# Performance work log

Measured on AMD Instinct MI355X. Metric: run time of the kernel, lower is better.

The kernel has to match this reference:

```python
import jax, jax.numpy as jnp
import numpy as np

B, L, D, F, E, K = 2, 2048, 1024, 4096, 8, 2


def setup_inputs() -> dict:
    key = jax.random.key(0)
    ks = jax.random.split(key, 8)
    s = 0.02
    return {
        "x": jax.random.normal(ks[0], (B, L, D), dtype=jnp.float32),
        "Wg": jax.random.normal(ks[1], (D, E), dtype=jnp.float32) * s,
        "bg": jnp.zeros((E,), dtype=jnp.float32),
        "W1": jax.random.normal(ks[2], (E, D, F), dtype=jnp.float32) * s,
        "b1": jnp.zeros((E, F), dtype=jnp.float32),
        "W2": jax.random.normal(ks[3], (E, F, D), dtype=jnp.float32) * s,
        "b2": jnp.zeros((E, D), dtype=jnp.float32),
    }


def reference(x, Wg, bg, W1, b1, W2, b2):
    num_experts = Wg.shape[1]
    gate_scores = x @ Wg + bg                                # [B,L,E]
    topk_scores, topk_ids = jax.lax.top_k(gate_scores, K)    # [B,L,K]
    topk_weights = jax.nn.softmax(topk_scores, axis=-1)      # [B,L,K]
    gate_probs = jax.nn.softmax(gate_scores, axis=-1)        # [B,L,E]

    onehot = jax.nn.one_hot(topk_ids, num_experts, dtype=x.dtype)  # [B,L,K,E]
    expert_mask = onehot.sum(axis=2)                         # [B,L,E]
    freq = expert_mask.mean(axis=(0, 1))                     # [E]
    prob_mean = gate_probs.mean(axis=(0, 1))                 # [E]
    load_balance_loss = num_experts * jnp.sum(freq * prob_mean)

    # combine weight per token per expert (0 if expert not selected)
    combine = jnp.sum(onehot * topk_weights[..., None], axis=2)    # [B,L,E]

    # dense dispatch: run every expert FFN on all tokens, weight & combine
    h = jnp.einsum('bld,edf->belf', x, W1) + b1[None, :, None, :]  # [B,E,L,F]
    h = jax.nn.gelu(h, approximate=False)                          # exact GELU (torch default)
    y = jnp.einsum('belf,efd->beld', h, W2) + b2[None, :, None, :] # [B,E,L,D]
    out = jnp.einsum('ble,beld->bld', combine, y)                  # [B,L,D]
    return out, load_balance_loss
```

## Files before the change

kernel.cpp:

```cpp
#include <hip/hip_runtime.h>
#include <hip/hip_bf16.h>
#include <cstdint>
#include <cstddef>

#define B_ 2
#define L_ 2048
#define D_ 1024
#define F_ 4096
#define E_ 8
#define NTOK 4096
#define MAXROWS 9216
#define MAXMT 72

typedef __hip_bfloat16 bf16;
typedef __attribute__((ext_vector_type(8))) short short8;
typedef __attribute__((ext_vector_type(4))) float floatx4;

typedef const __attribute__((address_space(1))) uint32_t* gptr_t;
typedef __attribute__((address_space(3))) uint32_t* lptr_t;

__device__ __forceinline__ void async_load16(const bf16* gp, bf16* lp) {
    __builtin_amdgcn_global_load_lds((gptr_t)(const void*)gp, (lptr_t)(void*)lp, 16, 0, 0);
}

__device__ __forceinline__ uint16_t bfbits(bf16 h) {
    union { bf16 b; uint16_t u; } v; v.b = h; return v.u;
}
__device__ __forceinline__ uint32_t pack2(float a, float b) {
    return (uint32_t)bfbits(__float2bfloat16(a)) | ((uint32_t)bfbits(__float2bfloat16(b)) << 16);
}
__device__ __forceinline__ float ublo(uint32_t u){ return __uint_as_float(u << 16); }
__device__ __forceinline__ float ubhi(uint32_t u){ return __uint_as_float(u & 0xffff0000u); }

__device__ __forceinline__ float fast_gelu(float x) {
    float x2 = x * x;
    float z = x * fmaf(0.1029432f, x2, 2.3022081f);
    z = fminf(z, 120.f);
    float u = __builtin_amdgcn_exp2f(z);
    return x * u * __builtin_amdgcn_rcpf(1.f + u);
}

__global__ __launch_bounds__(256) void gate_kernel(
    const float* __restrict__ x, const float* __restrict__ Wg,
    const float* __restrict__ bg, float* __restrict__ psum_pad,
    uint32_t* __restrict__ top_ids, float* __restrict__ top_w)
{
    __shared__ float psum_l[E_];
    int t = threadIdx.x;
    if (t < E_) psum_l[t] = 0.f;
    __syncthreads();

    int wave = t >> 6, lane = t & 63;
    for (int j = 0; j < 4; ++j) {
        int token = blockIdx.x * 16 + wave * 4 + j;
        const float* xr = x + (size_t)token * D_;

        float acc[E_];
#pragma unroll
        for (int e = 0; e < E_; ++e) acc[e] = 0.f;
#pragma unroll
        for (int i = 0; i < 4; ++i) {
            int d = lane * 4 + 256 * i;
            float4 xv = *(const float4*)(xr + d);
            const float* xs = &xv.x;
#pragma unroll
            for (int jj = 0; jj < 4; ++jj) {
                const float4* wr4 = (const float4*)(Wg + (size_t)(d + jj) * E_);
                float4 wa = wr4[0], wb = wr4[1];
                float xvj = xs[jj];
                acc[0] += xvj * wa.x;  acc[1] += xvj * wa.y;
                acc[2] += xvj * wa.z;  acc[3] += xvj * wa.w;
                acc[4] += xvj * wb.x;  acc[5] += xvj * wb.y;
                acc[6] += xvj * wb.z;  acc[7] += xvj * wb.w;
            }
        }
#pragma unroll
        for (int off = 32; off >= 1; off >>= 1) {
#pragma unroll
            for (int e = 0; e < E_; ++e) acc[e] += __shfl_xor(acc[e], off, 64);
        }
        if (lane == 0) {
            float s[E_];
#pragma unroll
            for (int e = 0; e < E_; ++e) s[e] = acc[e] + bg[e];
            int i0 = 0;
#pragma unroll
            for (int e = 1; e < E_; ++e) if (s[e] > s[i0]) i0 = e;
            int i1 = -1;
#pragma unroll
            for (int e = 0; e < E_; ++e) {
                if (e == i0) continue;
                if (i1 < 0 || s[e] > s[i1]) i1 = e;
            }
            float e1 = expf(s[i1] - s[i0]);
            float w0 = 1.f / (1.f + e1);
            float w1 = e1 * w0;
            top_ids[token] = (uint32_t)i0 | ((uint32_t)i1 << 8);
            top_w[token]        = w0;
            top_w[NTOK + token] = w1;

            float mx = s[i0], p[E_], sum = 0.f;
#pragma unroll
            for (int e = 0; e < E_; ++e) { p[e] = expf(s[e] - mx); sum += p[e]; }
            float inv = 1.f / sum;
#pragma unroll
            for (int e = 0; e < E_; ++e) atomicAdd(&psum_l[e], p[e] * inv);
        }
    }
    __syncthreads();
    if (t < E_) atomicAdd(&psum_pad[t * 32], psum_l[t]);
}

__global__ __launch_bounds__(256) void compact_kernel(
    const uint32_t* __restrict__ top_ids, const float* __restrict__ top_w,
    int* __restrict__ cnt, int* __restrict__ tok_list, float* __restrict__ w_list,
    int* __restrict__ rowid)
{
    int e = blockIdx.x;
    int t = threadIdx.x, wave = t >> 6, lane = t & 63;
    __shared__ int wcnt[4];
    int base = 0;
    for (int r0 = 0; r0 < NTOK; r0 += 256) {
        int token = r0 + t;
        uint32_t ids = top_ids[token];
        int slot = -1;
        if ((int)(ids & 255u) == e) slot = 0;
        else if ((int)((ids >> 8) & 255u) == e) slot = 1;
        unsigned long long mask = __ballot(slot >= 0);
        int lpos = __popcll(mask & ((1ull << lane) - 1ull));
        if (lane == 0) wcnt[wave] = (int)__popcll(mask);
        __syncthreads();
        int woff = 0, tot = 0;
#pragma unroll
        for (int w2 = 0; w2 < 4; ++w2) { if (w2 < wave) woff += wcnt[w2]; tot += wcnt[w2]; }
        if (slot >= 0) {
            int pos = base + woff + lpos;
            tok_list[e*NTOK + pos] = token;
            w_list[e*NTOK + pos]   = top_w[slot*NTOK + token];
            rowid[slot*NTOK + token] = (e << 13) | pos;
        }
        base += tot;
        __syncthreads();
    }
    if (t == 0) cnt[e] = base;
}

__global__ void finalize_gate_kernel(const int* __restrict__ cnt, const float* __restrict__ psum_pad,
                                     int* __restrict__ off, float* __restrict__ loss_out,
                                     int* __restrict__ mt_map, int* __restrict__ mt_hdr)
{
    int o = 0; float Ls = 0.f; int g = 0;
    for (int e = 0; e < E_; ++e) {
        off[e] = o;
        int mt = (cnt[e] + 127) >> 7;
        for (int m = 0; m < mt; ++m) mt_map[g++] = (e << 8) | m;
        o += mt << 7;
        Ls += (float)cnt[e] * psum_pad[e * 32];
    }
    mt_hdr[0] = g;
    mt_hdr[1] = (g + 7) >> 3;
    loss_out[0] = (float)E_ * Ls / ((float)NTOK * (float)NTOK);
}

__global__ __launch_bounds__(256) void transpose_bf16_kernel(
    const float* __restrict__ in, bf16* __restrict__ outp, int R, int C)
{
    int tilesR = R >> 6, tilesC = C >> 6;
    int per = tilesR * tilesC;
    int bx = blockIdx.x;
    int e  = bx / per; int r2 = bx % per;
    int tr = r2 / tilesC, tc = r2 % tilesC;
    int r0 = tr << 6, c0 = tc << 6;
    const float* ip = in  + (size_t)e * R * C;
    bf16*        op = outp + (size_t)e * R * C;

    __shared__ uint32_t T[64][36];
    int t = threadIdx.x;
    int rp = t >> 4;
    int c4 = (t & 15) * 4;

#pragma unroll
    for (int it = 0; it < 2; ++it) {
        int pr = rp + 16 * it;
        const float* p = ip + (size_t)(r0 + 2*pr) * C + c0 + c4;
        float4 a = *(const float4*)(p);
        float4 b = *(const float4*)(p + C);
        T[c4+0][pr] = pack2(a.x, b.x);
        T[c4+1][pr] = pack2(a.y, b.y);
        T[c4+2][pr] = pack2(a.z, b.z);
        T[c4+3][pr] = pack2(a.w, b.w);
    }
    __syncthreads();

    int s     = t & 7;
    int cbase = t >> 3;
#pragma unroll
    for (int pass = 0; pass < 2; ++pass) {
        int cc = cbase + 32 * pass;
        uint4 u = *(const uint4*)&T[cc][4*s];
        *(uint4*)(op + (size_t)(c0 + cc) * R + r0 + 8*s) = u;
    }
}

__global__ __launch_bounds__(256) void gather_kernel(
    const float* __restrict__ x, const int* __restrict__ cnt, const int* __restrict__ off,
    const int* __restrict__ tok_list, bf16* __restrict__ Xg)
{
    int bx = blockIdx.x;
    int e  = bx >> 12;
    int i  = bx & 4095;
    if (i >= cnt[e]) return;
    int tok = tok_list[e*NTOK + i];
    size_t row = (size_t)(off[e] + i);
    int t = threadIdx.x;
    float4 v = *(const float4*)(x + (size_t)tok * D_ + t*4);
    uint2 uu;
    uu.x = pack2(v.x, v.y);
    uu.y = pack2(v.z, v.w);
    *(uint2*)(Xg + row * D_ + t*4) = uu;
}

__global__ __launch_bounds__(256) void gemm1_kernel(
    const bf16* __restrict__ Xg, const bf16* __restrict__ W1t,
    const float* __restrict__ b1, const int* __restrict__ cnt,
    const int* __restrict__ off, bf16* __restrict__ H)
{
    int bx = blockIdx.x;
    int e  = bx >> 10;
    int r2 = bx & 1023;
    int mtile = r2 >> 5, ntile = r2 & 31;
    int n = cnt[e];
    if (mtile * 128 >= n) return;
    int row0 = off[e] + mtile * 128;
    int f0 = ntile * 128;

    __shared__ bf16 As[128*64];
    __shared__ bf16 Bs[128*64];

    int t = threadIdx.x;
    int wave = t >> 6, lane = t & 63;
    int wm = wave & 1, wn = wave >> 1;
    int q = lane >> 4, ln = lane & 15;
    int sm = lane >> 3, sc = lane & 7;

    const bf16* Abase = Xg  + (size_t)row0 * D_;
    const bf16* Bbase = W1t + ((size_t)e * F_ + f0) * D_;

    floatx4 acc[4][4];
#pragma unroll
    for (int mt = 0; mt < 4; ++mt)
#pragma unroll
        for (int nt = 0; nt < 4; ++nt) acc[mt][nt] = {0.f, 0.f, 0.f, 0.f};

    for (int kt = 0; kt < D_; kt += 64) {
        __syncthreads();
#pragma unroll
        for (int i = 0; i < 4; ++i) {
            int g = wave*4 + i;
            int m = g*8 + sm;
            int ca = sc ^ (m & 7);
            async_load16(Abase + (size_t)m * D_ + kt + ca*8, &As[g*512]);
            async_load16(Bbase + (size_t)m * D_ + kt + ca*8, &Bs[g*512]);
        }
        __syncthreads();
#pragma unroll
        for (int kk = 0; kk < 2; ++kk) {
            short8 av[4], bv[4];
#pragma unroll
            for (int mt = 0; mt < 4; ++mt) {
                int r = wm*64 + mt*16 + ln;
                int cs = (kk*4 + q) ^ (r & 7);
                av[mt] = *(const short8*)&As[r*64 + cs*8];
            }
#pragma unroll
            for (int nt = 0; nt < 4; ++nt) {
                int r = wn*64 + nt*16 + ln;
                int cs = (kk*4 + q) ^ (r & 7);
                bv[nt] = *(const short8*)&Bs[r*64 + cs*8];
            }
#pragma unroll
            for (int mt = 0; mt < 4; ++mt)
#pragma unroll
                for (int nt = 0; nt < 4; ++nt)
                    acc[mt][nt] = __builtin_amdgcn_mfma_f32_16x16x32_bf16(av[mt], bv[nt], acc[mt][nt], 0, 0, 0);
        }
    }

#pragma unroll
    for (int nt = 0; nt < 4; ++nt) {
        int f = f0 + wn*64 + nt*16 + ln;
        float b1v = b1[(size_t)e * F_ + f];
#pragma unroll
        for (int mt = 0; mt < 4; ++mt) {
            int rl = wm*64 + mt*16 + q*4;
#pragma unroll
            for (int r = 0; r < 4; ++r) {
                float v = acc[mt][nt][r] + b1v;
                H[(size_t)(row0 + rl + r) * F_ + f] = __float2bfloat16(fast_gelu(v));
            }
        }
    }
}

__global__ __launch_bounds__(256) void gemm2_kernel(
    const bf16* __restrict__ H, const bf16* __restrict__ W2t,
    const float* __restrict__ b2, const int* __restrict__ cnt, const int* __restrict__ off,
    const int* __restrict__ mt_map, const int* __restrict__ mt_hdr,
    bf16* __restrict__ Y)
{
    int bx = blockIdx.x;
    int k  = bx & 7;
    int j  = bx >> 3;
    int jj = j >> 3;
    int ntile = j & 7;
    int nmt = mt_hdr[0], qc = mt_hdr[1];
    if (jj >= qc) return;
    int mt = k * qc + jj;
    if (mt >= nmt) return;
    int em = mt_map[mt];
    int e = em >> 8, mtile = em & 255;
    int n = cnt[e];
    int row0 = off[e] + mtile * 128;
    int d0 = ntile * 128;

    __shared__ bf16 As[2][128*64];
    __shared__ bf16 Bs[2][128*64];

    int t = threadIdx.x;
    int wave = t >> 6, lane = t & 63;
    int wm = wave & 1, wn = wave >> 1;
    int q = lane >> 4, ln = lane & 15;
    int sm = lane >> 3, sc = lane & 7;

    const bf16* Abase = H   + (size_t)row0 * F_;
    const bf16* Bbase = W2t + ((size_t)e * D_ + d0) * F_;

    int g0 = wave*4;
    auto stage = [&](int b, int kt) {
#pragma unroll
        for (int i = 0; i < 4; ++i) {
            int g = g0 + i;
            int m = g*8 + sm;
            int ca = sc ^ (m & 7);
            async_load16(Abase + (size_t)m * F_ + kt + ca*8, &As[b][g*512]);
            async_load16(Bbase + (size_t)m * F_ + kt + ca*8, &Bs[b][g*512]);
        }
    };

    floatx4 acc[4][4];
#pragma unroll
    for (int mt2 = 0; mt2 < 4; ++mt2)
#pragma unroll
        for (int nt = 0; nt < 4; ++nt) acc[mt2][nt] = {0.f, 0.f, 0.f, 0.f};

    stage(0, 0);
    __syncthreads();
    int cur = 0;

    for (int kt = 0; kt < F_; kt += 64) {
        if (kt + 64 < F_) stage(cur ^ 1, kt + 64);
#pragma unroll
        for (int kk = 0; kk < 2; ++kk) {
            short8 av[4], bv[4];
#pragma unroll
            for (int mt2 = 0; mt2 < 4; ++mt2) {
                int r = wm*64 + mt2*16 + ln;
                int cs = (kk*4 + q) ^ (r & 7);
                av[mt2] = *(const short8*)&As[cur][r*64 + cs*8];
            }
#pragma unroll
            for (int nt = 0; nt < 4; ++nt) {
                int r = wn*64 + nt*16 + ln;
                int cs = (kk*4 + q) ^ (r & 7);
                bv[nt] = *(const short8*)&Bs[cur][r*64 + cs*8];
            }
#pragma unroll
            for (int mt2 = 0; mt2 < 4; ++mt2)
#pragma unroll
                for (int nt = 0; nt < 4; ++nt)
                    acc[mt2][nt] = __builtin_amdgcn_mfma_f32_16x16x32_bf16(av[mt2], bv[nt], acc[mt2][nt], 0, 0, 0);
        }
        __syncthreads();
        cur ^= 1;
    }

    float b2v[4];
#pragma unroll
    for (int nt = 0; nt < 4; ++nt)
        b2v[nt] = b2[(size_t)e * D_ + d0 + wn*64 + nt*16 + ln];

#pragma unroll
    for (int mt2 = 0; mt2 < 4; ++mt2) {
#pragma unroll
        for (int r = 0; r < 4; ++r) {
            int loc = wm*64 + mt2*16 + q*4 + r;
            int i = mtile*128 + loc;
            if (i < n) {
                bf16* yp = Y + (size_t)(row0 + loc) * D_ + d0;
#pragma unroll
                for (int nt = 0; nt < 4; ++nt)
                    yp[wn*64 + nt*16 + ln] = __float2bfloat16(acc[mt2][nt][r] + b2v[nt]);
            }
        }
    }
}

__global__ __launch_bounds__(256) void combine_kernel(
    const bf16* __restrict__ Y, const int* __restrict__ rowid,
    const float* __restrict__ top_w, const int* __restrict__ off,
    float* __restrict__ out)
{
    int tok = blockIdx.x;
    int t = threadIdx.x;
    int v0 = rowid[tok], v1 = rowid[NTOK + tok];
    float w0 = top_w[tok], w1 = top_w[NTOK + tok];
    size_t r0 = (size_t)(off[v0 >> 13] + (v0 & 8191));
    size_t r1 = (size_t)(off[v1 >> 13] + (v1 & 8191));
    uint2 a = *(const uint2*)(Y + r0 * D_ + t*4);
    uint2 b = *(const uint2*)(Y + r1 * D_ + t*4);
    float4 o;
    o.x = w0 * ublo(a.x) + w1 * ublo(b.x);
    o.y = w0 * ubhi(a.x) + w1 * ubhi(b.x);
    o.z = w0 * ublo(a.y) + w1 * ublo(b.y);
    o.w = w0 * ubhi(a.y) + w1 * ubhi(b.y);
    *(float4*)(out + (size_t)tok * D_ + t*4) = o;
}

extern "C" void kernel_launch(void* const* d_in, const int* in_sizes, int n_in,
                              void* d_out, int out_size, void* d_ws, size_t ws_size,
                              hipStream_t stream)
{
    const float* x  = (const float*)d_in[0];
    const float* Wg = (const float*)d_in[1];
    const float* bg = (const float*)d_in[2];
    const float* W1 = (const float*)d_in[3];
    const float* b1 = (const float*)d_in[4];
    const float* W2 = (const float*)d_in[5];
    const float* b2 = (const float*)d_in[6];
    float* out = (float*)d_out;

    char* ws = (char*)d_ws;
    int*      cnt      = (int*)(ws + 0);
    int*      off      = (int*)(ws + 128);
    int*      mt_map   = (int*)(ws + 256);
    int*      mt_hdr   = (int*)(ws + 576);
    float*    psum_pad = (float*)(ws + 1024);
    uint32_t* top_ids  = (uint32_t*)(ws + 8192);
    float*    top_w    = (float*)(ws + 8192 + 16384);
    int*      tok_list = (int*)(ws + 65536);
    float*    w_list   = (float*)(ws + 65536 + 131072);
    int*      rowid    = (int*)(ws + 327680);
    size_t o = 1u << 20;
    bf16*  W1t = (bf16*)(ws + o);  o += (size_t)E_ * D_ * F_ * 2;
    bf16*  W2t = (bf16*)(ws + o);  o += (size_t)E_ * F_ * D_ * 2;
    bf16*  Xg  = (bf16*)(ws + o);  o += (size_t)MAXROWS * D_ * 2;
    bf16*  H   = (bf16*)(ws + o);
    bf16*  Y   = Xg;

    hipMemsetAsync(ws + 1024, 0, 1024, stream);

    transpose_bf16_kernel<<<E_ * 16 * 64, 256, 0, stream>>>(W1, W1t, D_, F_);
    transpose_bf16_kernel<<<E_ * 64 * 16, 256, 0, stream>>>(W2, W2t, F_, D_);

    gate_kernel<<<256, 256, 0, stream>>>(x, Wg, bg, psum_pad, top_ids, top_w);
    compact_kernel<<<E_, 256, 0, stream>>>(top_ids, top_w, cnt, tok_list, w_list, rowid);
    finalize_gate_kernel<<<1, 1, 0, stream>>>(cnt, psum_pad, off, out + (size_t)NTOK * D_, mt_map, mt_hdr);
    gather_kernel<<<E_ * 4096, 256, 0, stream>>>(x, cnt, off, tok_list, Xg);

    gemm1_kernel<<<E_ * 32 * 32, 256, 0, stream>>>(Xg, W1t, b1, cnt, off, H);
    gemm2_kernel<<<MAXMT * 8, 256, 0, stream>>>(H, W2t, b2, cnt, off, mt_map, mt_hdr, Y);
    combine_kernel<<<NTOK, 256, 0, stream>>>(Y, rowid, top_w, off, out);
}
```

Measured before the change: 654.5 us.

## Add four-stage async LDS pipeline to both expert GEMMs and compact gemm1 grid

Both grouped GEMMs now keep four LDS buffers and issue async global-to-LDS loads three k-steps ahead. Explicit vmcnt waits and a single barrier per step replace the previous double-buffer or single-buffer schedule. gemm1 also takes the compacted m-tile map, so it launches only live tiles, interleaved across 8 slots the same way gemm2 does, instead of a fixed per-expert grid with early exits. Shared memory per block grows to 128KB, which limits occupancy to one block per CU, and the hand-counted vmcnt values depend on the exact number of loads per stage.

```diff
diff --git a/kernel.cpp b/kernel.cpp
--- a/kernel.cpp
+++ b/kernel.cpp
@@ -223,19 +223,25 @@
 __global__ __launch_bounds__(256) void gemm1_kernel(
     const bf16* __restrict__ Xg, const bf16* __restrict__ W1t,
     const float* __restrict__ b1, const int* __restrict__ cnt,
-    const int* __restrict__ off, bf16* __restrict__ H)
+    const int* __restrict__ off, const int* __restrict__ mt_map,
+    const int* __restrict__ mt_hdr, bf16* __restrict__ H)
 {
     int bx = blockIdx.x;
-    int e  = bx >> 10;
-    int r2 = bx & 1023;
-    int mtile = r2 >> 5, ntile = r2 & 31;
-    int n = cnt[e];
-    if (mtile * 128 >= n) return;
+    int k  = bx & 7;
+    int j  = bx >> 3;
+    int jj = j >> 5;
+    int ntile = j & 31;
+    int nmt = mt_hdr[0], qc = mt_hdr[1];
+    if (jj >= qc) return;
+    int mt = k * qc + jj;
+    if (mt >= nmt) return;
+    int em = mt_map[mt];
+    int e = em >> 8, mtile = em & 255;
     int row0 = off[e] + mtile * 128;
     int f0 = ntile * 128;
 
-    __shared__ bf16 As[128*64];
-    __shared__ bf16 Bs[128*64];
+    __shared__ bf16 As[4][128*64];
+    __shared__ bf16 Bs[4][128*64];
 
     int t = threadIdx.x;
     int wave = t >> 6, lane = t & 63;
@@ -246,56 +252,80 @@
     const bf16* Abase = Xg  + (size_t)row0 * D_;
     const bf16* Bbase = W1t + ((size_t)e * F_ + f0) * D_;
 
-    floatx4 acc[4][4];
-#pragma unroll
-    for (int mt = 0; mt < 4; ++mt)
-#pragma unroll
-        for (int nt = 0; nt < 4; ++nt) acc[mt][nt] = {0.f, 0.f, 0.f, 0.f};
-
-    for (int kt = 0; kt < D_; kt += 64) {
-        __syncthreads();
+    int g0 = wave*4;
+    auto stage = [&](int b, int kt) {
 #pragma unroll
         for (int i = 0; i < 4; ++i) {
-            int g = wave*4 + i;
+            int g = g0 + i;
             int m = g*8 + sm;
             int ca = sc ^ (m & 7);
-            async_load16(Abase + (size_t)m * D_ + kt + ca*8, &As[g*512]);
-            async_load16(Bbase + (size_t)m * D_ + kt + ca*8, &Bs[g*512]);
-        }
-        __syncthreads();
+            async_load16(Abase + (size_t)m * D_ + kt + ca*8, &As[b][g*512]);
+            async_load16(Bbase + (size_t)m * D_ + kt + ca*8, &Bs[b][g*512]);
+        }
+    };
+
+    floatx4 acc[4][4];
+#pragma unroll
+    for (int mt2 = 0; mt2 < 4; ++mt2)
+#pragma unroll
+        for (int nt = 0; nt < 4; ++nt) acc[mt2][nt] = {0.f, 0.f, 0.f, 0.f};
+
+    auto compute = [&](int b) {
 #pragma unroll
         for (int kk = 0; kk < 2; ++kk) {
             short8 av[4], bv[4];
 #pragma unroll
-            for (int mt = 0; mt < 4; ++mt) {
-                int r = wm*64 + mt*16 + ln;
+            for (int mt2 = 0; mt2 < 4; ++mt2) {
+                int r = wm*64 + mt2*16 + ln;
                 int cs = (kk*4 + q) ^ (r & 7);
-                av[mt] = *(const short8*)&As[r*64 + cs*8];
+                av[mt2] = *(const short8*)&As[b][r*64 + cs*8];
             }
 #pragma unroll
             for (int nt = 0; nt < 4; ++nt) {
                 int r = wn*64 + nt*16 + ln;
                 int cs = (kk*4 + q) ^ (r & 7);
-                bv[nt] = *(const short8*)&Bs[r*64 + cs*8];
-            }
-#pragma unroll
-            for (int mt = 0; mt < 4; ++mt)
+                bv[nt] = *(const short8*)&Bs[b][r*64 + cs*8];
+            }
+#pragma unroll
+            for (int mt2 = 0; mt2 < 4; ++mt2)
 #pragma unroll
                 for (int nt = 0; nt < 4; ++nt)
-                    acc[mt][nt] = __builtin_amdgcn_mfma_f32_16x16x32_bf16(av[mt], bv[nt], acc[mt][nt], 0, 0, 0);
-        }
-    }
+                    acc[mt2][nt] = __builtin_amdgcn_mfma_f32_16x16x32_bf16(av[mt2], bv[nt], acc[mt2][nt], 0, 0, 0);
+        }
+    };
+
+    const int NT = D_ / 64;
+    stage(0, 0); stage(1, 64); stage(2, 128);
+    for (int i = 0; i < NT - 3; ++i) {
+        asm volatile("s_waitcnt vmcnt(16)" ::: "memory");
+        __builtin_amdgcn_s_barrier();
+        __builtin_amdgcn_sched_barrier(0);
+        stage((i + 3) & 3, (i + 3) * 64);
+        compute(i & 3);
+    }
+    asm volatile("s_waitcnt vmcnt(16)" ::: "memory");
+    __builtin_amdgcn_s_barrier();
+    __builtin_amdgcn_sched_barrier(0);
+    compute((NT - 3) & 3);
+    asm volatile("s_waitcnt vmcnt(8)" ::: "memory");
+    __builtin_amdgcn_s_barrier();
+    __builtin_amdgcn_sched_barrier(0);
+    compute((NT - 2) & 3);
+    asm volatile("s_waitcnt vmcnt(0)" ::: "memory");
+    __builtin_amdgcn_s_barrier();
+    __builtin_amdgcn_sched_barrier(0);
+    compute((NT - 1) & 3);
 
 #pragma unroll
     for (int nt = 0; nt < 4; ++nt) {
         int f = f0 + wn*64 + nt*16 + ln;
         float b1v = b1[(size_t)e * F_ + f];
 #pragma unroll
-        for (int mt = 0; mt < 4; ++mt) {
-            int rl = wm*64 + mt*16 + q*4;
+        for (int mt2 = 0; mt2 < 4; ++mt2) {
+            int rl = wm*64 + mt2*16 + q*4;
 #pragma unroll
             for (int r = 0; r < 4; ++r) {
-                float v = acc[mt][nt][r] + b1v;
+                float v = acc[mt2][nt][r] + b1v;
                 H[(size_t)(row0 + rl + r) * F_ + f] = __float2bfloat16(fast_gelu(v));
             }
         }
@@ -323,8 +353,8 @@
     int row0 = off[e] + mtile * 128;
     int d0 = ntile * 128;
 
-    __shared__ bf16 As[2][128*64];
-    __shared__ bf16 Bs[2][128*64];
+    __shared__ bf16 As[4][128*64];
+    __shared__ bf16 Bs[4][128*64];
 
     int t = threadIdx.x;
     int wave = t >> 6, lane = t & 63;
@@ -353,12 +383,7 @@
 #pragma unroll
         for (int nt = 0; nt < 4; ++nt) acc[mt2][nt] = {0.f, 0.f, 0.f, 0.f};
 
-    stage(0, 0);
-    __syncthreads();
-    int cur = 0;
-
-    for (int kt = 0; kt < F_; kt += 64) {
-        if (kt + 64 < F_) stage(cur ^ 1, kt + 64);
+    auto compute = [&](int b) {
 #pragma unroll
         for (int kk = 0; kk < 2; ++kk) {
             short8 av[4], bv[4];
@@ -366,13 +391,13 @@
             for (int mt2 = 0; mt2 < 4; ++mt2) {
                 int r = wm*64 + mt2*16 + ln;
                 int cs = (kk*4 + q) ^ (r & 7);
-                av[mt2] = *(const short8*)&As[cur][r*64 + cs*8];
+                av[mt2] = *(const short8*)&As[b][r*64 + cs*8];
             }
 #pragma unroll
             for (int nt = 0; nt < 4; ++nt) {
                 int r = wn*64 + nt*16 + ln;
                 int cs = (kk*4 + q) ^ (r & 7);
-                bv[nt] = *(const short8*)&Bs[cur][r*64 + cs*8];
+                bv[nt] = *(const short8*)&Bs[b][r*64 + cs*8];
             }
 #pragma unroll
             for (int mt2 = 0; mt2 < 4; ++mt2)
@@ -380,9 +405,29 @@
                 for (int nt = 0; nt < 4; ++nt)
                     acc[mt2][nt] = __builtin_amdgcn_mfma_f32_16x16x32_bf16(av[mt2], bv[nt], acc[mt2][nt], 0, 0, 0);
         }
-        __syncthreads();
-        cur ^= 1;
-    }
+    };
+
+    const int NT = F_ / 64;
+    stage(0, 0); stage(1, 64); stage(2, 128);
+    for (int i = 0; i < NT - 3; ++i) {
+        asm volatile("s_waitcnt vmcnt(16)" ::: "memory");
+        __builtin_amdgcn_s_barrier();
+        __builtin_amdgcn_sched_barrier(0);
+        stage((i + 3) & 3, (i + 3) * 64);
+        compute(i & 3);
+    }
+    asm volatile("s_waitcnt vmcnt(16)" ::: "memory");
+    __builtin_amdgcn_s_barrier();
+    __builtin_amdgcn_sched_barrier(0);
+    compute((NT - 3) & 3);
+    asm volatile("s_waitcnt vmcnt(8)" ::: "memory");
+    __builtin_amdgcn_s_barrier();
+    __builtin_amdgcn_sched_barrier(0);
+    compute((NT - 2) & 3);
+    asm volatile("s_waitcnt vmcnt(0)" ::: "memory");
+    __builtin_amdgcn_s_barrier();
+    __builtin_amdgcn_sched_barrier(0);
+    compute((NT - 1) & 3);
 
     float b2v[4];
 #pragma unroll
@@ -467,7 +512,7 @@
     finalize_gate_kernel<<<1, 1, 0, stream>>>(cnt, psum_pad, off, out + (size_t)NTOK * D_, mt_map, mt_hdr);
     gather_kernel<<<E_ * 4096, 256, 0, stream>>>(x, cnt, off, tok_list, Xg);
 
-    gemm1_kernel<<<E_ * 32 * 32, 256, 0, stream>>>(Xg, W1t, b1, cnt, off, H);
+    gemm1_kernel<<<MAXMT * 32, 256, 0, stream>>>(Xg, W1t, b1, cnt, off, mt_map, mt_hdr, H);
     gemm2_kernel<<<MAXMT * 8, 256, 0, stream>>>(H, W2t, b2, cnt, off, mt_map, mt_hdr, Y);
     combine_kernel<<<NTOK, 256, 0, stream>>>(Y, rowid, top_w, off, out);
 }
```

New measurement: 810.0 us. 1.24x slower.
